# Performance work log

Measured on AMD Instinct MI355X. Metric: run time of the kernel, lower is better.

The kernel has to match this reference:

```python
import jax, jax.numpy as jnp
import numpy as np

N = 8192      # atoms
E = 131072    # edges (avg degree 16)
C = 32        # channels per irrep
Z = 10        # num_elements
G = 16        # num_graphs
NB = 8        # num_bessel
NSH = 9       # spherical harmonic components for max_ell=2 (1+3+5)
R_MAX = 5.0
P_CUT = 5     # num_polynomial_cutoff
AVG_NEIGH = 16.0
LMAP = np.array([0, 1, 1, 1, 2, 2, 2, 2, 2])  # m-component -> l index


def _sph(u):
    # real spherical harmonics up to l=2, 'component' normalization, unit input
    x, y, z = u[:, 0], u[:, 1], u[:, 2]
    s3, s5, s15 = 3.0 ** 0.5, 5.0 ** 0.5, 15.0 ** 0.5
    return jnp.stack([
        jnp.ones_like(x),
        s3 * x, s3 * y, s3 * z,
        s15 * x * y, s15 * y * z, (s5 / 2) * (3 * z * z - 1.0),
        s15 * x * z, (s15 / 2) * (x * x - y * y),
    ], axis=1)  # [E, 9]


def _radial(r):
    # Bessel radial basis with smooth polynomial cutoff (MACE RadialEmbeddingBlock)
    n = jnp.arange(1, NB + 1, dtype=r.dtype)  # [NB]
    pref = (2.0 / R_MAX) ** 0.5
    bessel = pref * jnp.sin(n[None, :] * jnp.pi * r[:, None] / R_MAX) / r[:, None]
    x = r / R_MAX
    p = float(P_CUT)
    env = (1.0 - (p + 1.0) * (p + 2.0) / 2.0 * x ** P_CUT
           + p * (p + 2.0) * x ** (P_CUT + 1)
           - p * (p + 1.0) / 2.0 * x ** (P_CUT + 2))
    env = env * (x < 1.0)
    return bessel * env[:, None]  # [E, NB]


def setup_inputs() -> dict:
    key = jax.random.key(0)
    k = jax.random.split(key, 24)
    positions = jax.random.normal(k[0], (N, 3), dtype=jnp.float32) * 2.0
    species = jax.random.randint(k[1], (N,), 0, Z)
    node_attrs = jax.nn.one_hot(species, Z, dtype=jnp.float32)
    edge_index = jax.random.randint(k[2], (2, E), 0, N, dtype=jnp.int32)
    batch = jnp.sort(jax.random.randint(k[3], (N,), 0, G, dtype=jnp.int32))
    charges = jax.random.normal(k[4], (N,), dtype=jnp.float32) * 0.1
    sd = 0.1
    atomic_energies = jax.random.normal(k[5], (Z,), dtype=jnp.float32)
    W_embed = jax.random.normal(k[6], (Z, C), dtype=jnp.float32) * sd
    R0 = jax.random.normal(k[7], (2, NB, 64), dtype=jnp.float32) / np.sqrt(NB)
    R1 = jax.random.normal(k[8], (2, 64, 64), dtype=jnp.float32) / 8.0
    R2 = jax.random.normal(k[9], (2, 64, 64), dtype=jnp.float32) / 8.0
    R3 = jax.random.normal(k[10], (2, 64, 3 * C), dtype=jnp.float32) / 8.0
    W_mix = jax.random.normal(k[11], (2, 3, C, C), dtype=jnp.float32) / np.sqrt(C)
    W_sc = jax.random.normal(k[12], (2, 3, C, C), dtype=jnp.float32) / np.sqrt(C)
    Wp1 = jax.random.normal(k[13], (2, Z, C), dtype=jnp.float32) * 0.5
    Wp2 = jax.random.normal(k[14], (2, Z, C), dtype=jnp.float32) * 0.5
    Wp3 = jax.random.normal(k[15], (2, Z, C), dtype=jnp.float32) * 0.5
    wE1 = jax.random.normal(k[16], (C,), dtype=jnp.float32) * sd
    wD1 = jax.random.normal(k[17], (C,), dtype=jnp.float32) * sd
    Wh = jax.random.normal(k[18], (C, 16), dtype=jnp.float32) / np.sqrt(C)
    wE2 = jax.random.normal(k[19], (16,), dtype=jnp.float32) * sd
    wD2 = jax.random.normal(k[20], (C,), dtype=jnp.float32) * sd
    return dict(positions=positions, node_attrs=node_attrs, charges=charges,
                atomic_energies=atomic_energies, W_embed=W_embed,
                R0=R0, R1=R1, R2=R2, R3=R3, W_mix=W_mix, W_sc=W_sc,
                Wp1=Wp1, Wp2=Wp2, Wp3=Wp3, wE1=wE1, wD1=wD1, Wh=Wh,
                wE2=wE2, wD2=wD2, edge_index=edge_index, batch=batch)


def reference(positions, node_attrs, charges, atomic_energies, W_embed,
              R0, R1, R2, R3, W_mix, W_sc, Wp1, Wp2, Wp3,
              wE1, wD1, Wh, wE2, wD2, edge_index, batch):
    snd, rcv = edge_index[0], edge_index[1]
    lmap = jnp.asarray(LMAP)

    # edge geometry
    vec = positions[rcv] - positions[snd]          # [E,3]
    r = jnp.sqrt(jnp.sum(vec * vec, axis=1) + 1e-12)
    Y = _sph(vec / r[:, None])                     # [E,9]
    rb = _radial(r)                                # [E,NB]

    # atomic reference energies e0
    node_e0 = node_attrs @ atomic_energies         # [N]
    e_tot = jax.ops.segment_sum(node_e0, batch, num_segments=G)

    # node embedding (scalar channels), lifted into full irrep layout [N,9,C]
    h0 = node_attrs @ W_embed
    h = jnp.zeros((N, NSH, C), h0.dtype).at[:, 0, :].set(h0)

    dip = jnp.zeros((N, 3), positions.dtype)
    for i in range(2):
        # radial MLP -> per-edge, per-l tensor-product weights
        x = jax.nn.silu(rb @ R0[i])
        x = jax.nn.silu(x @ R1[i])
        x = jax.nn.silu(x @ R2[i])
        Rw = (x @ R3[i]).reshape(E, 3, C)[:, lmap, :]       # [E,9,C]
        # edge-wise tensor product: scalar node feats x SH, radially weighted
        hs = h[:, 0, :]                                      # [N,C]
        msg = Rw * Y[:, :, None] * hs[snd][:, None, :]       # [E,9,C]
        # scatter-sum message passing
        A = jax.ops.segment_sum(msg, rcv, num_segments=N) / AVG_NEIGH
        A = jnp.einsum('nmc,mcd->nmd', A, W_mix[i][lmap])    # per-l linear
        sc = jnp.einsum('nmc,mcd->nmd', h, W_sc[i][lmap])    # self-connection
        # symmetric product basis (correlation 3, element-dependent weights)
        s = A[:, 0, :]
        w1 = node_attrs @ Wp1[i]
        w2 = node_attrs @ Wp2[i]
        w3 = node_attrs @ Wp3[i]
        B = A * (w1[:, None, :] + w2[:, None, :] * s[:, None, :]
                 + w3[:, None, :] * (s * s)[:, None, :])
        h = B + sc
        # readouts: energy from 0e channels, dipole from 1o channels
        if i == 0:
            e_node = h[:, 0, :] @ wE1
            d_node = jnp.einsum('nmc,c->nm', h[:, 1:4, :], wD1)
        else:
            hid = jax.nn.silu(h[:, 0, :] @ Wh)
            e_node = hid @ wE2
            d_node = jnp.einsum('nmc,c->nm', h[:, 1:4, :], wD2)
        e_tot = e_tot + jax.ops.segment_sum(e_node, batch, num_segments=G)
        dip = dip + d_node

    total_dipole = jax.ops.segment_sum(dip, batch, num_segments=G)
    total_dipole = total_dipole + jax.ops.segment_sum(
        charges[:, None] * positions, batch, num_segments=G)  # fixed-charge baseline
    return jnp.concatenate([e_tot[:, None], total_dipole], axis=1)  # [G,4]
```

## Files before the change

kernel.cpp:

```cpp
#include <hip/hip_runtime.h>
#include <math.h>

#define N_NODES 8192
#define N_EDGES 131072
#define C 32
#define Zn 10
#define NG 16
#define NB 8
#define H 64
#define TABN 4096
#define PPB 32
#define XS 73
#define NPB 8
#define CAP 64
#define SL 48

__device__ __forceinline__ float silu_f(float v){ return v / (1.0f + __expf(-v)); }

__global__ __launch_bounds__(256)
void prep_kernel(const float* __restrict__ pos, const int* __restrict__ ei,
                 int* __restrict__ cursor, int* __restrict__ bucket,
                 const float* __restrict__ na, const float* __restrict__ Wemb,
                 int* __restrict__ species, float* __restrict__ hg,
                 const float* __restrict__ R0g, const float* __restrict__ R1g,
                 const float* __restrict__ R2g, const float* __restrict__ R3g,
                 float2* __restrict__ Tab2){
  __shared__ float xsh[PPB*XS];
  int b = blockIdx.x;
  int tid = threadIdx.x;

  if (b >= 258){
    if (b < 770){
      int e = (b-258)*256 + tid;
      int snd = ei[e], rcv = ei[N_EDGES + e];
      float px = pos[rcv*3+0]-pos[snd*3+0];
      float py = pos[rcv*3+1]-pos[snd*3+1];
      float pz = pos[rcv*3+2]-pos[snd*3+2];
      float r2 = px*px+py*py+pz*pz;
      if (r2 < 25.0f){
        int slot = atomicAdd(cursor + rcv, 1);
        if (slot < CAP) bucket[rcv*CAP + slot] = snd;
      }
    } else {
      int n = (b-770)*256 + tid;
      int spec = 0;
      #pragma unroll
      for (int z = 1; z < Zn; z++) if (na[n*Zn+z] > 0.5f) spec = z;
      species[n] = spec;
      float4* hrow = (float4*)(hg + (size_t)n*288);
      const float4* wrow = (const float4*)(Wemb + spec*C);
      #pragma unroll
      for (int q = 0; q < 8; q++) hrow[q] = wrow[q];
      float4 z4 = make_float4(0.f,0.f,0.f,0.f);
      #pragma unroll
      for (int q = 8; q < 72; q++) hrow[q] = z4;
    }
    return;
  }

  int tb = b;
  const int nb = (TABN + PPB)/PPB;
  int half = tb / nb;
  int blk  = tb - half*nb;
  const float* R0i = R0g + half*NB*H;
  const float* R1i = R1g + half*H*H;
  const float* R2i = R2g + half*H*H;
  const float* R3i = R3g + half*H*96;
  float2* TabH = Tab2 + (size_t)half*((size_t)TABN*96);

  int pl = tid >> 3, jt = tid & 7;
  int i = blk*PPB + pl;
  float r = (i == 0) ? 1e-6f : (float)i * (5.0f/TABN);
  {
    float xr = r*0.2f;
    float env = 0.f;
    if (xr < 1.0f){
      float x2 = xr*xr, x5 = x2*x2*xr;
      env = 1.f - 21.f*x5 + 35.f*x5*xr - 15.f*x5*x2;
    }
    float sc = 0.6324555320336759f / r * env;
    xsh[pl*XS + jt] = sc * sinf((float)(jt+1)*0.6283185307179586f*r);
  }
  __syncthreads();

  float acc[12];
  #pragma unroll
  for (int j = 0; j < 8; j++) acc[j] = 0.f;
  #pragma unroll
  for (int k = 0; k < 8; k++){
    float xk = xsh[pl*XS + k];
    const float4* w4 = (const float4*)(R0i + k*H + jt*8);
    float4 wa = w4[0], wb = w4[1];
    acc[0]=fmaf(xk,wa.x,acc[0]); acc[1]=fmaf(xk,wa.y,acc[1]);
    acc[2]=fmaf(xk,wa.z,acc[2]); acc[3]=fmaf(xk,wa.w,acc[3]);
    acc[4]=fmaf(xk,wb.x,acc[4]); acc[5]=fmaf(xk,wb.y,acc[5]);
    acc[6]=fmaf(xk,wb.z,acc[6]); acc[7]=fmaf(xk,wb.w,acc[7]);
  }
  __syncthreads();
  #pragma unroll
  for (int j = 0; j < 8; j++) xsh[pl*XS + jt*8 + j] = silu_f(acc[j]);
  __syncthreads();

  const float* Wl[2] = {R1i, R2i};
  #pragma unroll
  for (int L = 0; L < 2; L++){
    const float* W = Wl[L];
    #pragma unroll
    for (int j = 0; j < 8; j++) acc[j] = 0.f;
    #pragma unroll 4
    for (int k = 0; k < H; k++){
      float xk = xsh[pl*XS + k];
      const float4* w4 = (const float4*)(W + k*H + jt*8);
      float4 wa = w4[0], wb = w4[1];
      acc[0]=fmaf(xk,wa.x,acc[0]); acc[1]=fmaf(xk,wa.y,acc[1]);
      acc[2]=fmaf(xk,wa.z,acc[2]); acc[3]=fmaf(xk,wa.w,acc[3]);
      acc[4]=fmaf(xk,wb.x,acc[4]); acc[5]=fmaf(xk,wb.y,acc[5]);
      acc[6]=fmaf(xk,wb.z,acc[6]); acc[7]=fmaf(xk,wb.w,acc[7]);
    }
    __syncthreads();
    #pragma unroll
    for (int j = 0; j < 8; j++) xsh[pl*XS + jt*8 + j] = silu_f(acc[j]);
    __syncthreads();
  }

  #pragma unroll
  for (int j = 0; j < 12; j++) acc[j] = 0.f;
  #pragma unroll 4
  for (int k = 0; k < H; k++){
    float xk = xsh[pl*XS + k];
    const float4* w4 = (const float4*)(R3i + k*96 + jt*12);
    float4 wa = w4[0], wb = w4[1], wc = w4[2];
    acc[0]=fmaf(xk,wa.x,acc[0]);  acc[1]=fmaf(xk,wa.y,acc[1]);
    acc[2]=fmaf(xk,wa.z,acc[2]);  acc[3]=fmaf(xk,wa.w,acc[3]);
    acc[4]=fmaf(xk,wb.x,acc[4]);  acc[5]=fmaf(xk,wb.y,acc[5]);
    acc[6]=fmaf(xk,wb.z,acc[6]);  acc[7]=fmaf(xk,wb.w,acc[7]);
    acc[8]=fmaf(xk,wc.x,acc[8]);  acc[9]=fmaf(xk,wc.y,acc[9]);
    acc[10]=fmaf(xk,wc.z,acc[10]); acc[11]=fmaf(xk,wc.w,acc[11]);
  }
  if (i <= TABN){
    int cb = jt*12;
    #pragma unroll
    for (int j = 0; j < 12; j++){
      int c = cb + j;
      float val = acc[j];
      if (i < TABN) TabH[(size_t)i*96 + c].x = val;
      if (i > 0)    TabH[(size_t)(i-1)*96 + c].y = val;
    }
  }
}

__global__ __launch_bounds__(512)
void node_kernel(const float2* __restrict__ Tab2, const int* __restrict__ bucket,
                 const int* __restrict__ deg,
                 const float* __restrict__ hg_in, float* __restrict__ hg_out,
                 const float* __restrict__ Wm_g, const float* __restrict__ Ws_g,
                 const float* __restrict__ Wp1, const float* __restrict__ Wp2,
                 const float* __restrict__ Wp3,
                 const int* __restrict__ species, const int* __restrict__ batch,
                 const float* __restrict__ ae, const float* __restrict__ charges,
                 const float* __restrict__ pos,
                 const float* __restrict__ wEv, const float* __restrict__ wDv,
                 const float* __restrict__ Whg, const float* __restrict__ wE2g,
                 int iter, float* __restrict__ out){
  __shared__ float WmT[3*32*34];
  __shared__ float WsT[3*32*34];
  __shared__ float abuf[NPB][288];
  __shared__ float sbuf[NPB][288];
  __shared__ float estage[NPB][SL][6];
  __shared__ float glds[NG][4];
  int tid = threadIdx.x;
  for (int t = tid; t < 3072; t += 512){
    int l = t >> 10, rem = t & 1023, c = rem >> 5, d = rem & 31;
    WmT[(l*32+d)*34 + c] = Wm_g[t];
    WsT[(l*32+d)*34 + c] = Ws_g[t];
  }
  if (tid < NG*4) glds[tid>>2][tid&3] = 0.f;
  int w = tid >> 6, lane = tid & 63;
  int c31 = lane & 31;
  bool hi = lane >= 32;
  int ng0 = blockIdx.x*NPB;
  int n = ng0 + w;

  int cnt = deg[n]; if (cnt > SL) cnt = SL;
  if (lane < cnt){
    int snd = bucket[n*CAP + lane];
    float px = pos[n*3+0] - pos[snd*3+0];
    float py = pos[n*3+1] - pos[snd*3+1];
    float pz = pos[n*3+2] - pos[snd*3+2];
    float r = sqrtf(px*px+py*py+pz*pz + 1e-12f);
    float inv = 1.0f/r;
    float* es = &estage[w][lane][0];
    es[0] = px*inv; es[1] = py*inv; es[2] = pz*inv;
    es[3] = r * (TABN/5.0f);
    es[4] = __int_as_float(snd);
  }

  const float s3 = 1.7320508075688772f;
  const float s5 = 2.23606797749979f;
  const float s15 = 3.872983346207417f;
  int colA = (hi ? 32 : 0) + c31;
  int colB = 32 + c31;
  int colC = 64 + c31;
  float acc0=0.f, acc1=0.f, acc2=0.f, acc3=0.f, acc4=0.f;
  #pragma unroll 4
  for (int j = 0; j < cnt; j++){
    const float* es = &estage[w][j][0];
    float x = es[0], y = es[1], z = es[2], u = es[3];
    int snd = __float_as_int(es[4]);
    int i0 = (int)u;
    if (i0 > TABN-1) i0 = TABN-1;
    float f = u - (float)i0;
    const float2* T2 = Tab2 + (size_t)i0*96;
    float hs = hg_in[(size_t)snd*288 + c31];
    float2 ta = T2[colA];
    float2 tb = T2[colB];
    float2 tc = T2[colC];
    float wv0 = fmaf(ta.y - ta.x, f, ta.x) * hs;
    float wv1 = fmaf(tb.y - tb.x, f, tb.x) * hs;
    float wv2 = fmaf(tc.y - tc.x, f, tc.x) * hs;
    float Ys0 = hi ? s3*x : 1.0f;
    float Ys1 = s3 * (hi ? z : y);
    float Ys2 = s15 * (hi ? y*z : x*y);
    float Ys3 = hi ? s15*x*z : 0.5f*s5*(3.f*z*z - 1.f);
    float Ys4 = 0.5f*s15*(x*x - y*y);
    acc0 = fmaf(wv0, Ys0, acc0);
    acc1 = fmaf(wv1, Ys1, acc1);
    acc2 = fmaf(wv2, Ys2, acc2);
    acc3 = fmaf(wv2, Ys3, acc3);
    acc4 = fmaf(wv2, Ys4, acc4);
  }
  abuf[w][lane]       = acc0 * (1.0f/16.0f);
  abuf[w][lane + 64]  = acc1 * (1.0f/16.0f);
  abuf[w][lane + 128] = acc2 * (1.0f/16.0f);
  abuf[w][lane + 192] = acc3 * (1.0f/16.0f);
  if (!hi) abuf[w][lane + 256] = acc4 * (1.0f/16.0f);
  __syncthreads();

  float a2[NPB], scv[NPB];
  int idx0 = w*64 + lane;
  bool actm = (w < 5) && (idx0 < 288);
  if (w < 5){
    int m = idx0 >> 5; if (m > 8) m = 8;
    int l = (m >= 4) ? 2 : ((m >= 1) ? 1 : 0);
    const float* wmB = WmT + (l*32 + c31)*34;
    const float* wsB = WsT + (l*32 + c31)*34;
    #pragma unroll
    for (int n2 = 0; n2 < NPB; n2++){ a2[n2] = 0.f; scv[n2] = 0.f; }
    #pragma unroll
    for (int q = 0; q < 8; q++){
      float2 wa0 = *(const float2*)(wmB + 4*q);
      float2 wa1 = *(const float2*)(wmB + 4*q + 2);
      float2 sa0 = *(const float2*)(wsB + 4*q);
      float2 sa1 = *(const float2*)(wsB + 4*q + 2);
      #pragma unroll
      for (int n2 = 0; n2 < NPB; n2++){
        float4 av = *(const float4*)(&abuf[n2][m*32 + 4*q]);
        float4 hv = *(const float4*)(hg_in + (size_t)(ng0+n2)*288 + m*32 + 4*q);
        a2[n2] = fmaf(av.x, wa0.x, a2[n2]); a2[n2] = fmaf(av.y, wa0.y, a2[n2]);
        a2[n2] = fmaf(av.z, wa1.x, a2[n2]); a2[n2] = fmaf(av.w, wa1.y, a2[n2]);
        scv[n2] = fmaf(hv.x, sa0.x, scv[n2]); scv[n2] = fmaf(hv.y, sa0.y, scv[n2]);
        scv[n2] = fmaf(hv.z, sa1.x, scv[n2]); scv[n2] = fmaf(hv.w, sa1.y, scv[n2]);
      }
    }
  }
  __syncthreads();
  if (actm){
    #pragma unroll
    for (int n2 = 0; n2 < NPB; n2++){
      abuf[n2][idx0] = a2[n2];
      sbuf[n2][idx0] = scv[n2];
    }
  }
  __syncthreads();

  int spec = species[n];
  float sval = abuf[w][c31];
  float p1 = Wp1[spec*C+c31], p2 = Wp2[spec*C+c31], p3 = Wp3[spec*C+c31];
  float f = p1 + p2*sval + p3*sval*sval;
  #pragma unroll
  for (int it = 0; it < 5; it++){
    int idx = it*64 + lane;
    if (idx < 288){
      float hn = abuf[w][idx]*f + sbuf[w][idx];
      hg_out[(size_t)n*288 + idx] = hn;
      abuf[w][idx] = hn;
    }
  }

  int g = batch[n];
  float dv0 = 0.f, dv1 = 0.f, dv2 = 0.f, ev = 0.f;
  if (lane < 32){
    dv0 = abuf[w][32+lane]*wDv[lane];
    dv1 = abuf[w][64+lane]*wDv[lane];
    dv2 = abuf[w][96+lane]*wDv[lane];
  }
  if (iter == 0){
    if (lane < 32) ev = abuf[w][lane]*wEv[lane];
  } else {
    if (lane < 16){
      float hid = 0.f;
      #pragma unroll
      for (int c = 0; c < 32; c++) hid = fmaf(abuf[w][c], Whg[c*16+lane], hid);
      hid = silu_f(hid);
      ev = hid * wE2g[lane];
    }
  }
  #pragma unroll
  for (int off = 16; off >= 1; off >>= 1){
    ev  += __shfl_down(ev,  off);
    dv0 += __shfl_down(dv0, off);
    dv1 += __shfl_down(dv1, off);
    dv2 += __shfl_down(dv2, off);
  }
  if (lane == 0){
    if (iter == 0){
      ev += ae[spec];
      float q = charges[n];
      dv0 += q*pos[n*3+0];
      dv1 += q*pos[n*3+1];
      dv2 += q*pos[n*3+2];
    }
    atomicAdd(&glds[g][0], ev);
    atomicAdd(&glds[g][1], dv0);
    atomicAdd(&glds[g][2], dv1);
    atomicAdd(&glds[g][3], dv2);
  }
  __syncthreads();
  if (tid < NG*4){
    float v = glds[tid>>2][tid&3];
    if (v != 0.f) atomicAdd(out + tid, v);
  }
}

extern "C" void kernel_launch(void* const* d_in, const int* in_sizes, int n_in,
                              void* d_out, int out_size, void* d_ws, size_t ws_size,
                              hipStream_t stream){
  const float* positions       = (const float*)d_in[0];
  const float* node_attrs      = (const float*)d_in[1];
  const float* charges         = (const float*)d_in[2];
  const float* atomic_energies = (const float*)d_in[3];
  const float* W_embed         = (const float*)d_in[4];
  const float* R0              = (const float*)d_in[5];
  const float* R1              = (const float*)d_in[6];
  const float* R2              = (const float*)d_in[7];
  const float* R3              = (const float*)d_in[8];
  const float* W_mix           = (const float*)d_in[9];
  const float* W_sc            = (const float*)d_in[10];
  const float* Wp1             = (const float*)d_in[11];
  const float* Wp2             = (const float*)d_in[12];
  const float* Wp3             = (const float*)d_in[13];
  const float* wE1             = (const float*)d_in[14];
  const float* wD1             = (const float*)d_in[15];
  const float* Wh              = (const float*)d_in[16];
  const float* wE2             = (const float*)d_in[17];
  const float* wD2             = (const float*)d_in[18];
  const int*   edge_index      = (const int*)d_in[19];
  const int*   batch           = (const int*)d_in[20];
  float* out = (float*)d_out;

  char* wsp = (char*)d_ws;
  int*    bucket = (int*)wsp;    wsp += sizeof(int)*(size_t)N_NODES*CAP;
  float2* Tab2   = (float2*)wsp; wsp += sizeof(float2)*(size_t)2*TABN*96;
  float*  hg_a   = (float*)wsp;  wsp += sizeof(float)*(size_t)N_NODES*288;
  float*  hg_b   = (float*)wsp;  wsp += sizeof(float)*(size_t)N_NODES*288;
  int* cursor    = (int*)wsp;    wsp += sizeof(int)*N_NODES;
  int* species   = (int*)wsp;    wsp += sizeof(int)*N_NODES;

  hipMemsetAsync(d_out, 0, 64*sizeof(float), stream);
  hipMemsetAsync(cursor, 0, N_NODES*sizeof(int), stream);

  prep_kernel<<<802, 256, 0, stream>>>(positions, edge_index, cursor, bucket,
                                       node_attrs, W_embed, species, hg_a,
                                       R0, R1, R2, R3, Tab2);

  for (int i = 0; i < 2; i++){
    const float* hin  = (i == 0) ? hg_a : hg_b;
    float*       hout = (i == 0) ? hg_b : hg_a;
    node_kernel<<<N_NODES/NPB, 512, 0, stream>>>(Tab2 + (size_t)i*TABN*96, bucket,
                                               cursor, hin, hout,
                                               W_mix + i*3*C*C, W_sc + i*3*C*C,
                                               Wp1 + i*Zn*C, Wp2 + i*Zn*C, Wp3 + i*Zn*C,
                                               species, batch,
                                               atomic_energies, charges, positions,
                                               wE1, (i == 0) ? wD1 : wD2,
                                               Wh, wE2, i, out);
  }
}
```

Before: 211.3 us.

## Coalesce node init writes, drop LDS weight transposes, fold output memset into prep

Node init now works per block of 64 nodes, staging species in LDS and writing the hidden-state rows as contiguous float4 stores instead of strided per-thread rows. node_kernel no longer copies and transposes W_mix and W_sc into LDS; it reads them straight from global memory with lane-contiguous access, and it reuses sbuf as edge staging, both of which cut LDS use and may raise occupancy. The output memset moves into prep_kernel, removing one launch, and the radial MLP loops are unrolled further. The costs are an extra barrier, weight loads going through cache instead of LDS, and reordered prep blocks.

```diff
diff --git a/kernel.cpp b/kernel.cpp
--- a/kernel.cpp
+++ b/kernel.cpp
@@ -24,14 +24,38 @@
                  int* __restrict__ species, float* __restrict__ hg,
                  const float* __restrict__ R0g, const float* __restrict__ R1g,
                  const float* __restrict__ R2g, const float* __restrict__ R3g,
-                 float2* __restrict__ Tab2){
+                 float2* __restrict__ Tab2, float* __restrict__ out){
   __shared__ float xsh[PPB*XS];
+  __shared__ int spec_lds[64];
   int b = blockIdx.x;
   int tid = threadIdx.x;
 
   if (b >= 258){
-    if (b < 770){
-      int e = (b-258)*256 + tid;
+    if (b < 386){
+      int n0 = (b-258)*64;
+      if (tid < 64){
+        int n = n0 + tid;
+        int spec = 0;
+        #pragma unroll
+        for (int z = 1; z < Zn; z++) if (na[n*Zn+z] > 0.5f) spec = z;
+        species[n] = spec;
+        spec_lds[tid] = spec;
+      }
+      if (b == 258 && tid >= 64 && tid < 128) out[tid-64] = 0.f;
+      __syncthreads();
+      float4* dst = (float4*)(hg + (size_t)n0*288);
+      const float4 z4 = make_float4(0.f,0.f,0.f,0.f);
+      #pragma unroll
+      for (int it = 0; it < 18; it++){
+        int f = it*256 + tid;
+        int node = f / 72;
+        int q = f - node*72;
+        float4 v = z4;
+        if (q < 8) v = ((const float4*)(Wemb + spec_lds[node]*C))[q];
+        dst[f] = v;
+      }
+    } else {
+      int e = (b-386)*256 + tid;
       int snd = ei[e], rcv = ei[N_EDGES + e];
       float px = pos[rcv*3+0]-pos[snd*3+0];
       float py = pos[rcv*3+1]-pos[snd*3+1];
@@ -41,19 +65,6 @@
         int slot = atomicAdd(cursor + rcv, 1);
         if (slot < CAP) bucket[rcv*CAP + slot] = snd;
       }
-    } else {
-      int n = (b-770)*256 + tid;
-      int spec = 0;
-      #pragma unroll
-      for (int z = 1; z < Zn; z++) if (na[n*Zn+z] > 0.5f) spec = z;
-      species[n] = spec;
-      float4* hrow = (float4*)(hg + (size_t)n*288);
-      const float4* wrow = (const float4*)(Wemb + spec*C);
-      #pragma unroll
-      for (int q = 0; q < 8; q++) hrow[q] = wrow[q];
-      float4 z4 = make_float4(0.f,0.f,0.f,0.f);
-      #pragma unroll
-      for (int q = 8; q < 72; q++) hrow[q] = z4;
     }
     return;
   }
@@ -107,7 +118,7 @@
     const float* W = Wl[L];
     #pragma unroll
     for (int j = 0; j < 8; j++) acc[j] = 0.f;
-    #pragma unroll 4
+    #pragma unroll 8
     for (int k = 0; k < H; k++){
       float xk = xsh[pl*XS + k];
       const float4* w4 = (const float4*)(W + k*H + jt*8);
@@ -125,7 +136,7 @@
 
   #pragma unroll
   for (int j = 0; j < 12; j++) acc[j] = 0.f;
-  #pragma unroll 4
+  #pragma unroll 8
   for (int k = 0; k < H; k++){
     float xk = xsh[pl*XS + k];
     const float4* w4 = (const float4*)(R3i + k*96 + jt*12);
@@ -162,18 +173,11 @@
                  const float* __restrict__ wEv, const float* __restrict__ wDv,
                  const float* __restrict__ Whg, const float* __restrict__ wE2g,
                  int iter, float* __restrict__ out){
-  __shared__ float WmT[3*32*34];
-  __shared__ float WsT[3*32*34];
   __shared__ float abuf[NPB][288];
   __shared__ float sbuf[NPB][288];
-  __shared__ float estage[NPB][SL][6];
   __shared__ float glds[NG][4];
+  float* estage = &sbuf[0][0];
   int tid = threadIdx.x;
-  for (int t = tid; t < 3072; t += 512){
-    int l = t >> 10, rem = t & 1023, c = rem >> 5, d = rem & 31;
-    WmT[(l*32+d)*34 + c] = Wm_g[t];
-    WsT[(l*32+d)*34 + c] = Ws_g[t];
-  }
   if (tid < NG*4) glds[tid>>2][tid&3] = 0.f;
   int w = tid >> 6, lane = tid & 63;
   int c31 = lane & 31;
@@ -189,7 +193,7 @@
     float pz = pos[n*3+2] - pos[snd*3+2];
     float r = sqrtf(px*px+py*py+pz*pz + 1e-12f);
     float inv = 1.0f/r;
-    float* es = &estage[w][lane][0];
+    float* es = estage + (w*SL + lane)*6;
     es[0] = px*inv; es[1] = py*inv; es[2] = pz*inv;
     es[3] = r * (TABN/5.0f);
     es[4] = __int_as_float(snd);
@@ -204,7 +208,7 @@
   float acc0=0.f, acc1=0.f, acc2=0.f, acc3=0.f, acc4=0.f;
   #pragma unroll 4
   for (int j = 0; j < cnt; j++){
-    const float* es = &estage[w][j][0];
+    const float* es = estage + (w*SL + j)*6;
     float x = es[0], y = es[1], z = es[2], u = es[3];
     int snd = __float_as_int(es[4]);
     int i0 = (int)u;
@@ -229,6 +233,7 @@
     acc3 = fmaf(wv2, Ys3, acc3);
     acc4 = fmaf(wv2, Ys4, acc4);
   }
+  __syncthreads();
   abuf[w][lane]       = acc0 * (1.0f/16.0f);
   abuf[w][lane + 64]  = acc1 * (1.0f/16.0f);
   abuf[w][lane + 128] = acc2 * (1.0f/16.0f);
@@ -242,24 +247,24 @@
   if (w < 5){
     int m = idx0 >> 5; if (m > 8) m = 8;
     int l = (m >= 4) ? 2 : ((m >= 1) ? 1 : 0);
-    const float* wmB = WmT + (l*32 + c31)*34;
-    const float* wsB = WsT + (l*32 + c31)*34;
+    const float* wmB = Wm_g + l*1024 + c31;
+    const float* wsB = Ws_g + l*1024 + c31;
     #pragma unroll
     for (int n2 = 0; n2 < NPB; n2++){ a2[n2] = 0.f; scv[n2] = 0.f; }
     #pragma unroll
     for (int q = 0; q < 8; q++){
-      float2 wa0 = *(const float2*)(wmB + 4*q);
-      float2 wa1 = *(const float2*)(wmB + 4*q + 2);
-      float2 sa0 = *(const float2*)(wsB + 4*q);
-      float2 sa1 = *(const float2*)(wsB + 4*q + 2);
+      float w0 = wmB[(4*q+0)*32], w1 = wmB[(4*q+1)*32];
+      float w2 = wmB[(4*q+2)*32], w3 = wmB[(4*q+3)*32];
+      float t0 = wsB[(4*q+0)*32], t1 = wsB[(4*q+1)*32];
+      float t2 = wsB[(4*q+2)*32], t3 = wsB[(4*q+3)*32];
       #pragma unroll
       for (int n2 = 0; n2 < NPB; n2++){
         float4 av = *(const float4*)(&abuf[n2][m*32 + 4*q]);
         float4 hv = *(const float4*)(hg_in + (size_t)(ng0+n2)*288 + m*32 + 4*q);
-        a2[n2] = fmaf(av.x, wa0.x, a2[n2]); a2[n2] = fmaf(av.y, wa0.y, a2[n2]);
-        a2[n2] = fmaf(av.z, wa1.x, a2[n2]); a2[n2] = fmaf(av.w, wa1.y, a2[n2]);
-        scv[n2] = fmaf(hv.x, sa0.x, scv[n2]); scv[n2] = fmaf(hv.y, sa0.y, scv[n2]);
-        scv[n2] = fmaf(hv.z, sa1.x, scv[n2]); scv[n2] = fmaf(hv.w, sa1.y, scv[n2]);
+        a2[n2] = fmaf(av.x, w0, a2[n2]); a2[n2] = fmaf(av.y, w1, a2[n2]);
+        a2[n2] = fmaf(av.z, w2, a2[n2]); a2[n2] = fmaf(av.w, w3, a2[n2]);
+        scv[n2] = fmaf(hv.x, t0, scv[n2]); scv[n2] = fmaf(hv.y, t1, scv[n2]);
+        scv[n2] = fmaf(hv.z, t2, scv[n2]); scv[n2] = fmaf(hv.w, t3, scv[n2]);
       }
     }
   }
@@ -366,12 +371,11 @@
   int* cursor    = (int*)wsp;    wsp += sizeof(int)*N_NODES;
   int* species   = (int*)wsp;    wsp += sizeof(int)*N_NODES;
 
-  hipMemsetAsync(d_out, 0, 64*sizeof(float), stream);
   hipMemsetAsync(cursor, 0, N_NODES*sizeof(int), stream);
 
-  prep_kernel<<<802, 256, 0, stream>>>(positions, edge_index, cursor, bucket,
+  prep_kernel<<<898, 256, 0, stream>>>(positions, edge_index, cursor, bucket,
                                        node_attrs, W_embed, species, hg_a,
-                                       R0, R1, R2, R3, Tab2);
+                                       R0, R1, R2, R3, Tab2, out);
 
   for (int i = 0; i < 2; i++){
     const float* hin  = (i == 0) ? hg_a : hg_b;
```

After: 206.7 us. -2.2%, faster.
